# Kernel tuning notes

Measured on AMD Instinct MI355X. Metric: run time of the kernel, lower is better.

Reference implementation:

```python
import jax, jax.numpy as jnp
import numpy as np

WS = 8          # window_size
H = 4           # num_heads
C = 128         # embed_dim
D = C // H      # head_dim
L = WS * WS     # tokens per window
B = 4096        # batch * num_windows


def _make_rel_index(ws):
    coords = np.stack(np.meshgrid(np.arange(ws), np.arange(ws), indexing='ij'))  # [2,ws,ws]
    flat = coords.reshape(2, -1)                       # [2, L]
    rel = flat[:, :, None] - flat[:, None, :]          # [2, L, L]
    rel = rel.transpose(1, 2, 0) + ws - 1              # [L, L, 2]
    return (rel[..., 0] * (2 * ws - 1) + rel[..., 1]).astype(np.int32)  # [L, L]


def setup_inputs() -> dict:
    key = jax.random.key(0)
    ks = jax.random.split(key, 10)
    s = 0.02
    return {
        'query': jax.random.normal(ks[0], (B, L, C), jnp.float32),
        'Wq': jax.random.normal(ks[1], (C, C), jnp.float32) * s,
        'bq': jnp.zeros((C,), jnp.float32),
        'Wk': jax.random.normal(ks[2], (C, C), jnp.float32) * s,
        'bk': jnp.zeros((C,), jnp.float32),
        'Wv': jax.random.normal(ks[3], (C, C), jnp.float32) * s,
        'bv': jnp.zeros((C,), jnp.float32),
        'Wo': jax.random.normal(ks[4], (C, C), jnp.float32) * s,
        'bo': jnp.zeros((C,), jnp.float32),
        'bias_table': jax.random.normal(ks[5], ((2 * WS - 1) ** 2, H), jnp.float32) * s,
        'rel_index': jnp.asarray(_make_rel_index(WS)),
    }


def reference(query, Wq, bq, Wk, bk, Wv, bv, Wo, bo, bias_table, rel_index):
    scale = D ** -0.5
    # projections (torch Linear: x @ W.T + b)
    q = (query @ Wq.T + bq).reshape(B, L, H, D).transpose(0, 2, 1, 3)  # [B,H,L,D]
    k = (query @ Wk.T + bk).reshape(B, L, H, D).transpose(0, 2, 1, 3)
    v = (query @ Wv.T + bv).reshape(B, L, H, D).transpose(0, 2, 1, 3)
    attn = jnp.einsum('bhqd,bhkd->bhqk', q, k) * scale               # [B,H,L,L]
    bias = bias_table[rel_index]                                      # [L,L,H]
    attn = attn + bias.transpose(2, 0, 1)[None]                       # add RPB
    attn = jax.nn.softmax(attn, axis=-1)
    out = jnp.einsum('bhqk,bhkd->bqhd', attn, v).reshape(B, L, C)
    out = out @ Wo.T + bo
    return out
```

## Files before the change

kernel.cpp:

```cpp
#include <hip/hip_runtime.h>
#include <hip/hip_bf16.h>

typedef unsigned int u32;
typedef unsigned short u16;
typedef __attribute__((ext_vector_type(8))) short short8;
typedef __attribute__((ext_vector_type(4))) float f32x4;
typedef __attribute__((ext_vector_type(2))) u32 u32x2;

#define LOG2E 1.4426950408889634f
#define SCALE 0.17677669529663687f

__device__ __forceinline__ u16 f2bf(float f) {
    u32 u = __builtin_bit_cast(u32, f);
    u += 0x7FFFu + ((u >> 16) & 1u);
    return (u16)(u >> 16);
}

__device__ __forceinline__ int sw128(int r, int e) { return r * 128 + (e ^ ((r & 7) << 3)); }
__device__ __forceinline__ int sw64 (int r, int e) { return r * 64  + (e ^ ((r & 7) << 3)); }

__global__ __launch_bounds__(256) void prep_kernel(
    const float* __restrict__ Wq, const float* __restrict__ Wk,
    const float* __restrict__ Wv, const float* __restrict__ Wo,
    const float* __restrict__ bias_table, const int* __restrict__ rel_index,
    u16* __restrict__ wsW, float* __restrict__ wsB)
{
    int idx = blockIdx.x * 256 + threadIdx.x;
    if (idx < 16384) {
        wsW[idx]         = f2bf(Wq[idx] * (SCALE * LOG2E));
        wsW[16384 + idx] = f2bf(Wk[idx]);
        wsW[32768 + idx] = f2bf(Wv[idx]);
        wsW[49152 + idx] = f2bf(Wo[idx]);
        int h = idx >> 12, kk = (idx >> 6) & 63, q = idx & 63;
        wsB[idx] = bias_table[rel_index[q * 64 + kk] * 4 + h] * LOG2E;
    }
}

__global__ __launch_bounds__(256, 2) void wattn_kernel(
    const float* __restrict__ x,
    const float* __restrict__ bq, const float* __restrict__ bk,
    const float* __restrict__ bv, const float* __restrict__ bo,
    const u16* __restrict__ Wbf, const float* __restrict__ biasT,
    float* __restrict__ out)
{
    __shared__ u16 x_sm[64 * 128];
    __shared__ u16 q_sm[64 * 128];
    __shared__ u16 k_sm[64 * 128];
    __shared__ u16 vT_sm[128 * 64];

    const int b    = blockIdx.x;
    const int tid  = threadIdx.x;
    const int wid  = tid >> 6;
    const int lane = tid & 63;
    const int g    = lane >> 4;
    const int c    = lane & 15;

    {
        const float* xb = x + (size_t)b * 8192;
        #pragma unroll
        for (int it = 0; it < 8; ++it) {
            int idx = it * 1024 + tid * 4;
            float4 v = *(const float4*)(xb + idx);
            int row = idx >> 7, col = idx & 127;
            u32x2 wv;
            wv.x = f2bf(v.x) | ((u32)f2bf(v.y) << 16);
            wv.y = f2bf(v.z) | ((u32)f2bf(v.w) << 16);
            *(u32x2*)&x_sm[sw128(row, col)] = wv;
        }
    }
    __syncthreads();

    short8 xa[4][4];
    #pragma unroll
    for (int mt = 0; mt < 4; ++mt)
        #pragma unroll
        for (int kt = 0; kt < 4; ++kt)
            xa[mt][kt] = *(const short8*)&x_sm[sw128(16 * mt + c, 32 * kt + 8 * g)];

    #pragma unroll
    for (int jj = 0; jj < 6; ++jj) {
        int job = jj * 4 + wid;
        int p  = job >> 3;
        int nt = job & 7;
        const float* bp = (p == 0) ? bq : (p == 1) ? bk : bv;
        float bcol = bp[16 * nt + c];
        if (p == 0) bcol *= (SCALE * LOG2E);
        f32x4 acc[4];
        #pragma unroll
        for (int mt = 0; mt < 4; ++mt) { f32x4 t = {bcol, bcol, bcol, bcol}; acc[mt] = t; }
        const u16* W = Wbf + p * 16384;
        #pragma unroll
        for (int kt = 0; kt < 4; ++kt) {
            short8 bf = *(const short8*)(W + (16 * nt + c) * 128 + 32 * kt + 8 * g);
            #pragma unroll
            for (int mt = 0; mt < 4; ++mt)
                acc[mt] = __builtin_amdgcn_mfma_f32_16x16x32_bf16(xa[mt][kt], bf, acc[mt], 0, 0, 0);
        }
        if (p < 2) {
            u16* dst = (p == 0) ? q_sm : k_sm;
            #pragma unroll
            for (int mt = 0; mt < 4; ++mt)
                #pragma unroll
                for (int r = 0; r < 4; ++r)
                    dst[sw128(16 * mt + 4 * g + r, 16 * nt + c)] = f2bf(acc[mt][r]);
        } else {
            #pragma unroll
            for (int mt = 0; mt < 4; ++mt) {
                u32x2 wv;
                wv.x = f2bf(acc[mt][0]) | ((u32)f2bf(acc[mt][1]) << 16);
                wv.y = f2bf(acc[mt][2]) | ((u32)f2bf(acc[mt][3]) << 16);
                *(u32x2*)&vT_sm[sw64(16 * nt + c, 16 * mt + 4 * g)] = wv;
            }
        }
    }
    __syncthreads();

    const int d0 = 32 * wid;
    short8 ka[4], qb[4];
    #pragma unroll
    for (int t = 0; t < 4; ++t) {
        ka[t] = *(const short8*)&k_sm[sw128(16 * t + c, d0 + 8 * g)];
        qb[t] = *(const short8*)&q_sm[sw128(16 * t + c, d0 + 8 * g)];
    }
    f32x4 accP[4][4];
    const float* bT = biasT + wid * 4096;
    #pragma unroll
    for (int mt = 0; mt < 4; ++mt)
        #pragma unroll
        for (int nt = 0; nt < 4; ++nt) {
            f32x4 ci;
            #pragma unroll
            for (int r = 0; r < 4; ++r)
                ci[r] = bT[(16 * mt + 4 * g + r) * 64 + 16 * nt + c];
            accP[mt][nt] = __builtin_amdgcn_mfma_f32_16x16x32_bf16(ka[mt], qb[nt], ci, 0, 0, 0);
        }
    __syncthreads();

    #pragma unroll
    for (int nt = 0; nt < 4; ++nt) {
        float m = accP[0][nt][0];
        #pragma unroll
        for (int mt = 0; mt < 4; ++mt)
            #pragma unroll
            for (int r = 0; r < 4; ++r) m = fmaxf(m, accP[mt][nt][r]);
        m = fmaxf(m, __shfl_xor(m, 16, 64));
        m = fmaxf(m, __shfl_xor(m, 32, 64));
        float s = 0.f;
        #pragma unroll
        for (int mt = 0; mt < 4; ++mt)
            #pragma unroll
            for (int r = 0; r < 4; ++r) {
                float e = exp2f(accP[mt][nt][r] - m);
                accP[mt][nt][r] = e;
                s += e;
            }
        s += __shfl_xor(s, 16, 64);
        s += __shfl_xor(s, 32, 64);
        float rinv = 1.0f / s;
        #pragma unroll
        for (int mt = 0; mt < 4; ++mt)
            #pragma unroll
            for (int r = 0; r < 4; ++r) accP[mt][nt][r] *= rinv;
    }

    u16* Pw = ((wid & 2) ? k_sm : x_sm) + (wid & 1) * 4096;
    #pragma unroll
    for (int mt = 0; mt < 4; ++mt)
        #pragma unroll
        for (int nt = 0; nt < 4; ++nt) {
            u32x2 wv;
            wv.x = f2bf(accP[mt][nt][0]) | ((u32)f2bf(accP[mt][nt][1]) << 16);
            wv.y = f2bf(accP[mt][nt][2]) | ((u32)f2bf(accP[mt][nt][3]) << 16);
            *(u32x2*)&Pw[sw64(16 * nt + c, 16 * mt + 4 * g)] = wv;
        }

    f32x4 accO[2][4];
    #pragma unroll
    for (int mD = 0; mD < 2; ++mD)
        #pragma unroll
        for (int nt = 0; nt < 4; ++nt) { f32x4 z = {0.f, 0.f, 0.f, 0.f}; accO[mD][nt] = z; }
    #pragma unroll
    for (int kt = 0; kt < 2; ++kt) {
        short8 va[2];
        #pragma unroll
        for (int mD = 0; mD < 2; ++mD)
            va[mD] = *(const short8*)&vT_sm[sw64(d0 + 16 * mD + c, 32 * kt + 8 * g)];
        #pragma unroll
        for (int nt = 0; nt < 4; ++nt) {
            short8 pb = *(const short8*)&Pw[sw64(16 * nt + c, 32 * kt + 8 * g)];
            #pragma unroll
            for (int mD = 0; mD < 2; ++mD)
                accO[mD][nt] = __builtin_amdgcn_mfma_f32_16x16x32_bf16(va[mD], pb, accO[mD][nt], 0, 0, 0);
        }
    }

    #pragma unroll
    for (int mD = 0; mD < 2; ++mD)
        #pragma unroll
        for (int nt = 0; nt < 4; ++nt) {
            u32x2 wv;
            wv.x = f2bf(accO[mD][nt][0]) | ((u32)f2bf(accO[mD][nt][1]) << 16);
            wv.y = f2bf(accO[mD][nt][2]) | ((u32)f2bf(accO[mD][nt][3]) << 16);
            *(u32x2*)&q_sm[sw128(16 * nt + c, d0 + 16 * mD + 4 * g)] = wv;
        }
    __syncthreads();

    short8 ha[4][4];
    #pragma unroll
    for (int mt = 0; mt < 4; ++mt)
        #pragma unroll
        for (int kt = 0; kt < 4; ++kt)
            ha[mt][kt] = *(const short8*)&q_sm[sw128(16 * mt + c, 32 * kt + 8 * g)];
    const u16* Wo_ = Wbf + 3 * 16384;
    #pragma unroll
    for (int j = 0; j < 2; ++j) {
        int nt = wid * 2 + j;
        float bocol = bo[16 * nt + c];
        f32x4 acc[4];
        #pragma unroll
        for (int mt = 0; mt < 4; ++mt) { f32x4 t = {bocol, bocol, bocol, bocol}; acc[mt] = t; }
        #pragma unroll
        for (int kt = 0; kt < 4; ++kt) {
            short8 wf = *(const short8*)(Wo_ + (16 * nt + c) * 128 + 32 * kt + 8 * g);
            #pragma unroll
            for (int mt = 0; mt < 4; ++mt)
                acc[mt] = __builtin_amdgcn_mfma_f32_16x16x32_bf16(ha[mt][kt], wf, acc[mt], 0, 0, 0);
        }
        float* ob = out + (size_t)b * 8192;
        #pragma unroll
        for (int mt = 0; mt < 4; ++mt)
            #pragma unroll
            for (int r = 0; r < 4; ++r)
                ob[(16 * mt + 4 * g + r) * 128 + 16 * nt + c] = acc[mt][r];
    }
}

extern "C" void kernel_launch(void* const* d_in, const int* in_sizes, int n_in,
                              void* d_out, int out_size, void* d_ws, size_t ws_size,
                              hipStream_t stream)
{
    const float* query      = (const float*)d_in[0];
    const float* Wq         = (const float*)d_in[1];
    const float* bq         = (const float*)d_in[2];
    const float* Wk         = (const float*)d_in[3];
    const float* bk         = (const float*)d_in[4];
    const float* Wv         = (const float*)d_in[5];
    const float* bv         = (const float*)d_in[6];
    const float* Wo         = (const float*)d_in[7];
    const float* bo         = (const float*)d_in[8];
    const float* bias_table = (const float*)d_in[9];
    const int*   rel_index  = (const int*)d_in[10];

    u16*   wsW = (u16*)d_ws;
    float* wsB = (float*)((char*)d_ws + 131072);

    prep_kernel<<<dim3(64), dim3(256), 0, stream>>>(Wq, Wk, Wv, Wo, bias_table, rel_index, wsW, wsB);
    wattn_kernel<<<dim3(4096), dim3(256), 0, stream>>>(query, bq, bk, bv, bo, wsW, wsB, (float*)d_out);
}
```

Before: 119.0 us.

## Assign one head per wavefront, shrink shared memory, defer softmax normalization

Each wavefront now computes the Q/K/V projections for its own head and keeps the per-head Q, K, V^T tiles in a private 6144-element region of a single 48 KB shared buffer. This removes the block-wide barriers between projection and attention and cuts shared memory so three blocks can fit per CU (launch bounds raised to 3). The bias table is pre-permuted into MFMA accumulator layout so each lane loads it as one f32x4 vector. Softmax division is moved after the PV matmul, and float-to-bf16 conversion uses the library intrinsic. In exchange, register pressure rises under the tighter occupancy bound and each wave does more serial work.

```diff
diff --git a/kernel.cpp b/kernel.cpp
--- a/kernel.cpp
+++ b/kernel.cpp
@@ -11,9 +11,10 @@
 #define SCALE 0.17677669529663687f
 
 __device__ __forceinline__ u16 f2bf(float f) {
-    u32 u = __builtin_bit_cast(u32, f);
-    u += 0x7FFFu + ((u >> 16) & 1u);
-    return (u16)(u >> 16);
+    return __builtin_bit_cast(u16, __float2bfloat16(f));
+}
+__device__ __forceinline__ u32 pkbf(float a, float b) {
+    return (u32)f2bf(a) | ((u32)f2bf(b) << 16);
 }
 
 __device__ __forceinline__ int sw128(int r, int e) { return r * 128 + (e ^ ((r & 7) << 3)); }
@@ -31,22 +32,21 @@
         wsW[16384 + idx] = f2bf(Wk[idx]);
         wsW[32768 + idx] = f2bf(Wv[idx]);
         wsW[49152 + idx] = f2bf(Wo[idx]);
-        int h = idx >> 12, kk = (idx >> 6) & 63, q = idx & 63;
+        int h = idx >> 12, t = (idx >> 8) & 15, l = (idx >> 2) & 63, r = idx & 3;
+        int mt = t >> 2, nt = t & 3, g = l >> 4, c = l & 15;
+        int kk = 16 * mt + 4 * g + r, q = 16 * nt + c;
         wsB[idx] = bias_table[rel_index[q * 64 + kk] * 4 + h] * LOG2E;
     }
 }
 
-__global__ __launch_bounds__(256, 2) void wattn_kernel(
+__global__ __launch_bounds__(256, 3) void wattn_kernel(
     const float* __restrict__ x,
     const float* __restrict__ bq, const float* __restrict__ bk,
     const float* __restrict__ bv, const float* __restrict__ bo,
     const u16* __restrict__ Wbf, const float* __restrict__ biasT,
     float* __restrict__ out)
 {
-    __shared__ u16 x_sm[64 * 128];
-    __shared__ u16 q_sm[64 * 128];
-    __shared__ u16 k_sm[64 * 128];
-    __shared__ u16 vT_sm[128 * 64];
+    __shared__ u16 smem[24576];
 
     const int b    = blockIdx.x;
     const int tid  = threadIdx.x;
@@ -55,6 +55,9 @@
     const int g    = lane >> 4;
     const int c    = lane & 15;
 
+    u16* qk = smem + wid * 6144;
+    u16* vT = qk + 4096;
+
     {
         const float* xb = x + (size_t)b * 8192;
         #pragma unroll
@@ -63,9 +66,9 @@
             float4 v = *(const float4*)(xb + idx);
             int row = idx >> 7, col = idx & 127;
             u32x2 wv;
-            wv.x = f2bf(v.x) | ((u32)f2bf(v.y) << 16);
-            wv.y = f2bf(v.z) | ((u32)f2bf(v.w) << 16);
-            *(u32x2*)&x_sm[sw128(row, col)] = wv;
+            wv.x = pkbf(v.x, v.y);
+            wv.y = pkbf(v.z, v.w);
+            *(u32x2*)&smem[sw128(row, col)] = wv;
         }
     }
     __syncthreads();
@@ -75,67 +78,64 @@
     for (int mt = 0; mt < 4; ++mt)
         #pragma unroll
         for (int kt = 0; kt < 4; ++kt)
-            xa[mt][kt] = *(const short8*)&x_sm[sw128(16 * mt + c, 32 * kt + 8 * g)];
-
-    #pragma unroll
-    for (int jj = 0; jj < 6; ++jj) {
-        int job = jj * 4 + wid;
-        int p  = job >> 3;
-        int nt = job & 7;
+            xa[mt][kt] = *(const short8*)&smem[sw128(16 * mt + c, 32 * kt + 8 * g)];
+    __syncthreads();
+
+    const int h = wid, d0 = 32 * h;
+    #pragma unroll
+    for (int p = 0; p < 3; ++p) {
         const float* bp = (p == 0) ? bq : (p == 1) ? bk : bv;
-        float bcol = bp[16 * nt + c];
-        if (p == 0) bcol *= (SCALE * LOG2E);
-        f32x4 acc[4];
-        #pragma unroll
-        for (int mt = 0; mt < 4; ++mt) { f32x4 t = {bcol, bcol, bcol, bcol}; acc[mt] = t; }
-        const u16* W = Wbf + p * 16384;
-        #pragma unroll
-        for (int kt = 0; kt < 4; ++kt) {
-            short8 bf = *(const short8*)(W + (16 * nt + c) * 128 + 32 * kt + 8 * g);
-            #pragma unroll
-            for (int mt = 0; mt < 4; ++mt)
-                acc[mt] = __builtin_amdgcn_mfma_f32_16x16x32_bf16(xa[mt][kt], bf, acc[mt], 0, 0, 0);
-        }
-        if (p < 2) {
-            u16* dst = (p == 0) ? q_sm : k_sm;
-            #pragma unroll
-            for (int mt = 0; mt < 4; ++mt)
+        #pragma unroll
+        for (int j = 0; j < 2; ++j) {
+            int nt = 2 * h + j;
+            float bcol = bp[16 * nt + c];
+            if (p == 0) bcol *= (SCALE * LOG2E);
+            f32x4 acc[4];
+            #pragma unroll
+            for (int mt = 0; mt < 4; ++mt) { f32x4 t = {bcol, bcol, bcol, bcol}; acc[mt] = t; }
+            const u16* W = Wbf + p * 16384 + (16 * nt + c) * 128;
+            #pragma unroll
+            for (int kt = 0; kt < 4; ++kt) {
+                short8 bfr = *(const short8*)(W + 32 * kt + 8 * g);
                 #pragma unroll
-                for (int r = 0; r < 4; ++r)
-                    dst[sw128(16 * mt + 4 * g + r, 16 * nt + c)] = f2bf(acc[mt][r]);
-        } else {
-            #pragma unroll
-            for (int mt = 0; mt < 4; ++mt) {
-                u32x2 wv;
-                wv.x = f2bf(acc[mt][0]) | ((u32)f2bf(acc[mt][1]) << 16);
-                wv.y = f2bf(acc[mt][2]) | ((u32)f2bf(acc[mt][3]) << 16);
-                *(u32x2*)&vT_sm[sw64(16 * nt + c, 16 * mt + 4 * g)] = wv;
+                for (int mt = 0; mt < 4; ++mt)
+                    acc[mt] = __builtin_amdgcn_mfma_f32_16x16x32_bf16(xa[mt][kt], bfr, acc[mt], 0, 0, 0);
             }
-        }
-    }
-    __syncthreads();
-
-    const int d0 = 32 * wid;
+            if (p < 2) {
+                int colb = p * 32 + 16 * j + c;
+                #pragma unroll
+                for (int mt = 0; mt < 4; ++mt)
+                    #pragma unroll
+                    for (int r = 0; r < 4; ++r)
+                        qk[sw64(16 * mt + 4 * g + r, colb)] = f2bf(acc[mt][r]);
+            } else {
+                #pragma unroll
+                for (int mt = 0; mt < 4; ++mt) {
+                    u32x2 wv;
+                    wv.x = pkbf(acc[mt][0], acc[mt][1]);
+                    wv.y = pkbf(acc[mt][2], acc[mt][3]);
+                    *(u32x2*)&vT[sw64(16 * j + c, 16 * mt + 4 * g)] = wv;
+                }
+            }
+        }
+    }
+
     short8 ka[4], qb[4];
     #pragma unroll
     for (int t = 0; t < 4; ++t) {
-        ka[t] = *(const short8*)&k_sm[sw128(16 * t + c, d0 + 8 * g)];
-        qb[t] = *(const short8*)&q_sm[sw128(16 * t + c, d0 + 8 * g)];
+        qb[t] = *(const short8*)&qk[sw64(16 * t + c, 8 * g)];
+        ka[t] = *(const short8*)&qk[sw64(16 * t + c, 32 + 8 * g)];
     }
     f32x4 accP[4][4];
-    const float* bT = biasT + wid * 4096;
-    #pragma unroll
-    for (int mt = 0; mt < 4; ++mt)
-        #pragma unroll
-        for (int nt = 0; nt < 4; ++nt) {
-            f32x4 ci;
-            #pragma unroll
-            for (int r = 0; r < 4; ++r)
-                ci[r] = bT[(16 * mt + 4 * g + r) * 64 + 16 * nt + c];
-            accP[mt][nt] = __builtin_amdgcn_mfma_f32_16x16x32_bf16(ka[mt], qb[nt], ci, 0, 0, 0);
-        }
-    __syncthreads();
-
+    const f32x4* bT = (const f32x4*)(biasT + h * 4096);
+    #pragma unroll
+    for (int mt = 0; mt < 4; ++mt)
+        #pragma unroll
+        for (int nt = 0; nt < 4; ++nt)
+            accP[mt][nt] = __builtin_amdgcn_mfma_f32_16x16x32_bf16(
+                ka[mt], qb[nt], bT[(mt * 4 + nt) * 64 + lane], 0, 0, 0);
+
+    float rinv[4];
     #pragma unroll
     for (int nt = 0; nt < 4; ++nt) {
         float m = accP[0][nt][0];
@@ -156,22 +156,17 @@
             }
         s += __shfl_xor(s, 16, 64);
         s += __shfl_xor(s, 32, 64);
-        float rinv = 1.0f / s;
-        #pragma unroll
-        for (int mt = 0; mt < 4; ++mt)
-            #pragma unroll
-            for (int r = 0; r < 4; ++r) accP[mt][nt][r] *= rinv;
-    }
-
-    u16* Pw = ((wid & 2) ? k_sm : x_sm) + (wid & 1) * 4096;
+        rinv[nt] = 1.0f / s;
+    }
+
     #pragma unroll
     for (int mt = 0; mt < 4; ++mt)
         #pragma unroll
         for (int nt = 0; nt < 4; ++nt) {
             u32x2 wv;
-            wv.x = f2bf(accP[mt][nt][0]) | ((u32)f2bf(accP[mt][nt][1]) << 16);
-            wv.y = f2bf(accP[mt][nt][2]) | ((u32)f2bf(accP[mt][nt][3]) << 16);
-            *(u32x2*)&Pw[sw64(16 * nt + c, 16 * mt + 4 * g)] = wv;
+            wv.x = pkbf(accP[mt][nt][0], accP[mt][nt][1]);
+            wv.y = pkbf(accP[mt][nt][2], accP[mt][nt][3]);
+            *(u32x2*)&qk[sw64(16 * nt + c, 16 * mt + 4 * g)] = wv;
         }
 
     f32x4 accO[2][4];
@@ -184,24 +179,26 @@
         short8 va[2];
         #pragma unroll
         for (int mD = 0; mD < 2; ++mD)
-            va[mD] = *(const short8*)&vT_sm[sw64(d0 + 16 * mD + c, 32 * kt + 8 * g)];
+            va[mD] = *(const short8*)&vT[sw64(16 * mD + c, 32 * kt + 8 * g)];
         #pragma unroll
         for (int nt = 0; nt < 4; ++nt) {
-            short8 pb = *(const short8*)&Pw[sw64(16 * nt + c, 32 * kt + 8 * g)];
+            short8 pb = *(const short8*)&qk[sw64(16 * nt + c, 32 * kt + 8 * g)];
             #pragma unroll
             for (int mD = 0; mD < 2; ++mD)
                 accO[mD][nt] = __builtin_amdgcn_mfma_f32_16x16x32_bf16(va[mD], pb, accO[mD][nt], 0, 0, 0);
         }
     }
+    __syncthreads();
 
     #pragma unroll
     for (int mD = 0; mD < 2; ++mD)
         #pragma unroll
         for (int nt = 0; nt < 4; ++nt) {
+            float riv = rinv[nt];
             u32x2 wv;
-            wv.x = f2bf(accO[mD][nt][0]) | ((u32)f2bf(accO[mD][nt][1]) << 16);
-            wv.y = f2bf(accO[mD][nt][2]) | ((u32)f2bf(accO[mD][nt][3]) << 16);
-            *(u32x2*)&q_sm[sw128(16 * nt + c, d0 + 16 * mD + 4 * g)] = wv;
+            wv.x = pkbf(accO[mD][nt][0] * riv, accO[mD][nt][1] * riv);
+            wv.y = pkbf(accO[mD][nt][2] * riv, accO[mD][nt][3] * riv);
+            *(u32x2*)&smem[sw128(16 * nt + c, d0 + 16 * mD + 4 * g)] = wv;
         }
     __syncthreads();
 
@@ -210,23 +207,24 @@
     for (int mt = 0; mt < 4; ++mt)
         #pragma unroll
         for (int kt = 0; kt < 4; ++kt)
-            ha[mt][kt] = *(const short8*)&q_sm[sw128(16 * mt + c, 32 * kt + 8 * g)];
+            ha[mt][kt] = *(const short8*)&smem[sw128(16 * mt + c, 32 * kt + 8 * g)];
     const u16* Wo_ = Wbf + 3 * 16384;
+    float* ob = out + (size_t)b * 8192;
     #pragma unroll
     for (int j = 0; j < 2; ++j) {
-        int nt = wid * 2 + j;
+        int nt = 2 * wid + j;
         float bocol = bo[16 * nt + c];
         f32x4 acc[4];
         #pragma unroll
         for (int mt = 0; mt < 4; ++mt) { f32x4 t = {bocol, bocol, bocol, bocol}; acc[mt] = t; }
+        const u16* W = Wo_ + (16 * nt + c) * 128;
         #pragma unroll
         for (int kt = 0; kt < 4; ++kt) {
-            short8 wf = *(const short8*)(Wo_ + (16 * nt + c) * 128 + 32 * kt + 8 * g);
+            short8 wf = *(const short8*)(W + 32 * kt + 8 * g);
             #pragma unroll
             for (int mt = 0; mt < 4; ++mt)
                 acc[mt] = __builtin_amdgcn_mfma_f32_16x16x32_bf16(ha[mt][kt], wf, acc[mt], 0, 0, 0);
         }
-        float* ob = out + (size_t)b * 8192;
         #pragma unroll
         for (int mt = 0; mt < 4; ++mt)
             #pragma unroll
```

After: 127.7 us. +7.3%, slower.
